# Kernel optimization log

Measured on AMD Instinct MI355X. Metric: run time of the kernel, lower is better.

Reference implementation:

```python
import jax, jax.numpy as jnp
import numpy as np

N = 50000      # nodes
E = 1600000    # edges (avg degree 32)
F_IN = 3       # PROTEINS num_node_features
H = 64         # dim_h
G = 512        # num graphs in batch
C = 2          # PROTEINS num_classes
BN_EPS = 1e-5


def setup_inputs() -> dict:
    key = jax.random.key(0)
    ks = iter(jax.random.split(key, 64))

    def rn(shape, s=0.1):
        return (jax.random.normal(next(ks), shape) * s).astype(jnp.float32)

    inp = {"x": rn((N, F_IN), 1.0)}
    for li, din in ((1, F_IN), (2, H), (3, H)):
        p = f"conv{li}_"
        inp[p + "w1"] = rn((din, H))
        inp[p + "b1"] = rn((H,))
        inp[p + "bn_g"] = jnp.ones((H,), jnp.float32)
        inp[p + "bn_b"] = jnp.zeros((H,), jnp.float32)
        inp[p + "bn_m"] = rn((H,))
        inp[p + "bn_v"] = jax.random.uniform(next(ks), (H,), jnp.float32, 0.5, 1.5)
        inp[p + "w2"] = rn((H, H))
        inp[p + "b2"] = rn((H,))
    inp["lin1_w"] = rn((3 * H, 3 * H))
    inp["lin1_b"] = rn((3 * H,))
    inp["lin2_w"] = rn((3 * H, C))
    inp["lin2_b"] = rn((C,))
    inp["edge_index"] = jax.random.randint(next(ks), (2, E), 0, N, jnp.int64)
    inp["batch"] = jnp.sort(jax.random.randint(next(ks), (N,), 0, G, jnp.int64))
    return inp


def gin_conv(x, src, dst, w1, b1, g, bb, m, v, w2, b2):
    # GINConv, eps=0: mlp(x + sum_{j->i} x_j); aggregate messages at target (dst)
    agg = jax.ops.segment_sum(x[src], dst, num_segments=N)  # [N, d]
    h = x + agg
    h = h @ w1 + b1
    h = (h - m) * jax.lax.rsqrt(v + BN_EPS) * g + bb  # BatchNorm1d (eval)
    h = jax.nn.relu(h)
    h = jax.nn.relu(h @ w2 + b2)
    return h


def reference(x,
              conv1_w1, conv1_b1, conv1_bn_g, conv1_bn_b, conv1_bn_m, conv1_bn_v, conv1_w2, conv1_b2,
              conv2_w1, conv2_b1, conv2_bn_g, conv2_bn_b, conv2_bn_m, conv2_bn_v, conv2_w2, conv2_b2,
              conv3_w1, conv3_b1, conv3_bn_g, conv3_bn_b, conv3_bn_m, conv3_bn_v, conv3_w2, conv3_b2,
              lin1_w, lin1_b, lin2_w, lin2_b,
              edge_index, batch):
    src, dst = edge_index[0], edge_index[1]
    h1 = gin_conv(x,  src, dst, conv1_w1, conv1_b1, conv1_bn_g, conv1_bn_b, conv1_bn_m, conv1_bn_v, conv1_w2, conv1_b2)
    h2 = gin_conv(h1, src, dst, conv2_w1, conv2_b1, conv2_bn_g, conv2_bn_b, conv2_bn_m, conv2_bn_v, conv2_w2, conv2_b2)
    h3 = gin_conv(h2, src, dst, conv3_w1, conv3_b1, conv3_bn_g, conv3_bn_b, conv3_bn_m, conv3_bn_v, conv3_w2, conv3_b2)
    # global_add_pool per graph
    p1 = jax.ops.segment_sum(h1, batch, num_segments=G)
    p2 = jax.ops.segment_sum(h2, batch, num_segments=G)
    p3 = jax.ops.segment_sum(h3, batch, num_segments=G)
    h = jnp.concatenate((p1, p2, p3), axis=1)          # [G, 3H]
    h = jax.nn.relu(h @ lin1_w + lin1_b)
    # dropout p=0.5 is identity in eval mode
    h = h @ lin2_w + lin2_b                            # [G, C]
    return (h, jax.nn.log_softmax(h, axis=1))
```

## Files before the change

### kernel.cpp

```cpp
#include <hip/hip_runtime.h>
#include <hip/hip_bf16.h>
#include <math.h>

#define N_NODES 50000
#define N_EDGES 1600000
#define H 64
#define G_GRAPHS 512
#define C_CLS 2
#define BN_EPS 1e-5f
#define NBUCK 196
#define E4 (N_EDGES / 4)
#define CSR_BLOCKS ((E4 + 511) / 512)

typedef __attribute__((ext_vector_type(8))) short short8;
typedef __attribute__((ext_vector_type(4))) float floatx4;

__device__ __forceinline__ float bflo(unsigned int u) { return __uint_as_float(u << 16); }
__device__ __forceinline__ float bfhi(unsigned int u) { return __uint_as_float(u & 0xffff0000u); }
__device__ __forceinline__ unsigned int bf16_rne(float f) {
    unsigned int u = __float_as_uint(f);
    u += 0x7fffu + ((u >> 16) & 1u);
    return u >> 16;
}

__global__ __launch_bounds__(256) void pack_x_kernel(const float* __restrict__ x,
                                                     uint2* __restrict__ xb) {
    int node = blockIdx.x * blockDim.x + threadIdx.x;
    if (node >= N_NODES) return;
    uint2 p;
    p.x = bf16_rne(x[node * 3 + 0]) | (bf16_rne(x[node * 3 + 1]) << 16);
    p.y = bf16_rne(x[node * 3 + 2]);
    xb[node] = p;
}

__global__ __launch_bounds__(256) void bhist_kernel(const int* __restrict__ dst,
                                                    int* __restrict__ gbh) {
    __shared__ int bh[NBUCK];
    int t = threadIdx.x;
    if (t < NBUCK) bh[t] = 0;
    __syncthreads();
    int base = blockIdx.x * 512;
#pragma unroll
    for (int p = 0; p < 2; p++) {
        int i = base + p * 256 + t;
        if (i < E4) {
            int4 d = ((const int4*)dst)[i];
            atomicAdd(&bh[d.x >> 8], 1);
            atomicAdd(&bh[d.y >> 8], 1);
            atomicAdd(&bh[d.z >> 8], 1);
            atomicAdd(&bh[d.w >> 8], 1);
        }
    }
    __syncthreads();
    if (t < NBUCK && bh[t]) atomicAdd(&gbh[t], bh[t]);
}

__global__ __launch_bounds__(256) void bscan_kernel(const int* __restrict__ gbh,
                                                    int* __restrict__ bucket_start,
                                                    int* __restrict__ cursor,
                                                    int* __restrict__ row_start) {
    __shared__ int s[256];
    int t = threadIdx.x;
    int v = (t < NBUCK) ? gbh[t] : 0;
    s[t] = v;
    __syncthreads();
    for (int off = 1; off < 256; off <<= 1) {
        int u = 0;
        if (t >= off) u = s[t - off];
        __syncthreads();
        if (t >= off) s[t] += u;
        __syncthreads();
    }
    int excl = s[t] - v;
    if (t < NBUCK) { bucket_start[t] = excl; cursor[t] = excl; }
    if (t == 0) { bucket_start[NBUCK] = N_EDGES; row_start[N_NODES] = N_EDGES; }
}

__global__ __launch_bounds__(256) void bscatter_kernel(const int* __restrict__ src,
                                                       const int* __restrict__ dst,
                                                       int* __restrict__ cursor,
                                                       int* __restrict__ gpacked) {
    __shared__ int bh[NBUCK];
    int t = threadIdx.x;
    if (t < NBUCK) bh[t] = 0;
    __syncthreads();
    int base = blockIdx.x * 512;

    int pkA[4], bkA[4], lrA[4]; bool vA = false;
    int pkB[4], bkB[4], lrB[4]; bool vB = false;
    {
        int i = base + t;
        if (i < E4) {
            vA = true;
            int4 s4 = ((const int4*)src)[i];
            int4 d4 = ((const int4*)dst)[i];
            bkA[0] = d4.x >> 8; pkA[0] = ((d4.x & 255) << 16) | s4.x; lrA[0] = atomicAdd(&bh[bkA[0]], 1);
            bkA[1] = d4.y >> 8; pkA[1] = ((d4.y & 255) << 16) | s4.y; lrA[1] = atomicAdd(&bh[bkA[1]], 1);
            bkA[2] = d4.z >> 8; pkA[2] = ((d4.z & 255) << 16) | s4.z; lrA[2] = atomicAdd(&bh[bkA[2]], 1);
            bkA[3] = d4.w >> 8; pkA[3] = ((d4.w & 255) << 16) | s4.w; lrA[3] = atomicAdd(&bh[bkA[3]], 1);
        }
    }
    {
        int i = base + 256 + t;
        if (i < E4) {
            vB = true;
            int4 s4 = ((const int4*)src)[i];
            int4 d4 = ((const int4*)dst)[i];
            bkB[0] = d4.x >> 8; pkB[0] = ((d4.x & 255) << 16) | s4.x; lrB[0] = atomicAdd(&bh[bkB[0]], 1);
            bkB[1] = d4.y >> 8; pkB[1] = ((d4.y & 255) << 16) | s4.y; lrB[1] = atomicAdd(&bh[bkB[1]], 1);
            bkB[2] = d4.z >> 8; pkB[2] = ((d4.z & 255) << 16) | s4.z; lrB[2] = atomicAdd(&bh[bkB[2]], 1);
            bkB[3] = d4.w >> 8; pkB[3] = ((d4.w & 255) << 16) | s4.w; lrB[3] = atomicAdd(&bh[bkB[3]], 1);
        }
    }
    __syncthreads();
    if (t < NBUCK) {
        int c = bh[t];
        bh[t] = c ? atomicAdd(&cursor[t], c) : 0;
    }
    __syncthreads();
    if (vA) {
#pragma unroll
        for (int q = 0; q < 4; q++) gpacked[bh[bkA[q]] + lrA[q]] = pkA[q];
    }
    if (vB) {
#pragma unroll
        for (int q = 0; q < 4; q++) gpacked[bh[bkB[q]] + lrB[q]] = pkB[q];
    }
}

__global__ __launch_bounds__(256) void bcsr_kernel(const int* __restrict__ gpacked,
                                                   const int* __restrict__ bucket_start,
                                                   int* __restrict__ row_start,
                                                   int* __restrict__ edge_src) {
    __shared__ int cnt[256];
    __shared__ int pref[256];
    int b = blockIdx.x;
    int t = threadIdx.x;
    int bs = bucket_start[b], be = bucket_start[b + 1];
    cnt[t] = 0;
    __syncthreads();
    for (int i = bs + t; i < be; i += 256) atomicAdd(&cnt[gpacked[i] >> 16], 1);
    __syncthreads();
    int v = cnt[t];
    pref[t] = v;
    __syncthreads();
    for (int off = 1; off < 256; off <<= 1) {
        int u = 0;
        if (t >= off) u = pref[t - off];
        __syncthreads();
        if (t >= off) pref[t] += u;
        __syncthreads();
    }
    int excl = pref[t] - v;
    int node = b * 256 + t;
    if (node < N_NODES) row_start[node] = bs + excl;
    cnt[t] = excl;
    __syncthreads();
    for (int i = bs + t; i < be; i += 256) {
        int p = gpacked[i];
        int pos = atomicAdd(&cnt[p >> 16], 1);
        edge_src[bs + pos] = p & 0xffff;
    }
}

__global__ __launch_bounds__(512) void gather3_mid_kernel(
    const float* __restrict__ x, const uint2* __restrict__ xb,
    const int* __restrict__ row_start, const int* __restrict__ edge_src,
    const float* __restrict__ w1, const float* __restrict__ b1,
    const float* __restrict__ bn_g, const float* __restrict__ bn_b,
    const float* __restrict__ bn_m, const float* __restrict__ bn_v,
    __hip_bfloat16* __restrict__ mid) {
    int tid = threadIdx.x;
    int wave = tid >> 6;
    int j = tid & 63;
    int node = blockIdx.x * 8 + wave;

    int rs = row_start[node], re = row_start[node + 1];
    float a0 = 0.f, a1 = 0.f, a2 = 0.f;
    for (int t = rs + j; t < re; t += 64) {
        uint2 p = xb[edge_src[t]];
        a0 += bflo(p.x);
        a1 += bfhi(p.x);
        a2 += bflo(p.y);
    }
#pragma unroll
    for (int off = 32; off > 0; off >>= 1) {
        a0 += __shfl_xor(a0, off);
        a1 += __shfl_xor(a1, off);
        a2 += __shfl_xor(a2, off);
    }
    float in0 = a0 + x[node * 3 + 0];
    float in1 = a1 + x[node * 3 + 1];
    float in2 = a2 + x[node * 3 + 2];

    float sc = rsqrtf(bn_v[j] + BN_EPS) * bn_g[j];
    float sh = bn_b[j] - bn_m[j] * sc;
    float m = b1[j] + in0 * w1[j] + in1 * w1[H + j] + in2 * w1[2 * H + j];
    m = fmaxf(m * sc + sh, 0.f);
    ((unsigned short*)mid)[(size_t)node * H + j] = (unsigned short)bf16_rne(m);
}

#define IOP 72
__global__ __launch_bounds__(256) void matmul2_mfma_kernel(
    const __hip_bfloat16* __restrict__ xin,
    const float* __restrict__ w2, const float* __restrict__ b2,
    __hip_bfloat16* __restrict__ hout) {
    __shared__ unsigned short s_w2t[H * IOP];
    __shared__ unsigned short s_out[4][16 * IOP];

    int tid = threadIdx.x;
    for (int idx = tid; idx < H * H; idx += 256) {
        int k = idx >> 6, jj = idx & 63;
        s_w2t[jj * IOP + k] = (unsigned short)bf16_rne(w2[idx]);
    }
    int lane = tid & 63, wave = tid >> 6;
    int quad = lane >> 4, l15 = lane & 15;
    float bb2[4];
#pragma unroll
    for (int jt = 0; jt < 4; jt++) bb2[jt] = b2[jt * 16 + l15];
    __syncthreads();

    int base = blockIdx.x * 64 + wave * 16;
    const unsigned short* xr = (const unsigned short*)xin;
    int am = min(base + l15, N_NODES - 1);
    short8 a0 = *(const short8*)(xr + (size_t)am * H + quad * 8);
    short8 a1 = *(const short8*)(xr + (size_t)am * H + quad * 8 + 32);

    unsigned short* outw = s_out[wave];
#pragma unroll
    for (int jt = 0; jt < 4; jt++) {
        short8 b0 = *(const short8*)&s_w2t[(jt * 16 + l15) * IOP + quad * 8];
        short8 bv = *(const short8*)&s_w2t[(jt * 16 + l15) * IOP + quad * 8 + 32];
        floatx4 c = {0.f, 0.f, 0.f, 0.f};
        c = __builtin_amdgcn_mfma_f32_16x16x32_bf16(a0, b0, c, 0, 0, 0);
        c = __builtin_amdgcn_mfma_f32_16x16x32_bf16(a1, bv, c, 0, 0, 0);
#pragma unroll
        for (int r = 0; r < 4; r++) {
            float v = fmaxf(c[r] + bb2[jt], 0.f);
            outw[(quad * 4 + r) * IOP + jt * 16 + l15] = (unsigned short)bf16_rne(v);
        }
    }
    __syncthreads();

    unsigned short* ho = (unsigned short*)hout;
#pragma unroll
    for (int cc = 0; cc < 2; cc++) {
        int r = cc * 8 + (lane >> 3);
        int node = base + r;
        if (node < N_NODES) {
            short8 v = *(const short8*)&outw[r * IOP + (lane & 7) * 8];
            *(short8*)(ho + (size_t)node * H + (lane & 7) * 8) = v;
        }
    }
}

__global__ __launch_bounds__(512) void gather_kernel(
    const __hip_bfloat16* __restrict__ hin, const int* __restrict__ row_start,
    const int* __restrict__ edge_src, __hip_bfloat16* __restrict__ xs) {
    int tid = threadIdx.x;
    int wave = tid >> 6;
    int j = tid & 63;
    int o = j >> 3;
    int jo = j & 7;
    int node = blockIdx.x * 8 + wave;

    const char* hb = (const char*)hin;
    int rs = row_start[node], re = row_start[node + 1];
    float a0 = 0.f, a1 = 0.f, a2 = 0.f, a3 = 0.f, a4 = 0.f, a5 = 0.f, a6 = 0.f, a7 = 0.f;
    for (int base = rs; base < re; base += 64) {
        int idx = base + j;
        int sv = (idx < re) ? edge_src[idx] : 0;
        int cnt = min(64, re - base);
        int i = 0;
        for (; i + 8 <= cnt; i += 8) {
            int s = __shfl(sv, i + o);
            uint4 raw = *(const uint4*)(hb + (size_t)s * 128 + jo * 16);
            a0 += bflo(raw.x); a1 += bfhi(raw.x);
            a2 += bflo(raw.y); a3 += bfhi(raw.y);
            a4 += bflo(raw.z); a5 += bfhi(raw.z);
            a6 += bflo(raw.w); a7 += bfhi(raw.w);
        }
        if (i < cnt) {
            int r = cnt - i;
            int s = __shfl(sv, i + (o < r ? o : 0));
            uint4 raw = *(const uint4*)(hb + (size_t)s * 128 + jo * 16);
            if (o < r) {
                a0 += bflo(raw.x); a1 += bfhi(raw.x);
                a2 += bflo(raw.y); a3 += bfhi(raw.y);
                a4 += bflo(raw.z); a5 += bfhi(raw.z);
                a6 += bflo(raw.w); a7 += bfhi(raw.w);
            }
        }
    }
    a0 += __shfl_xor(a0, 8); a0 += __shfl_xor(a0, 16); a0 += __shfl_xor(a0, 32);
    a1 += __shfl_xor(a1, 8); a1 += __shfl_xor(a1, 16); a1 += __shfl_xor(a1, 32);
    a2 += __shfl_xor(a2, 8); a2 += __shfl_xor(a2, 16); a2 += __shfl_xor(a2, 32);
    a3 += __shfl_xor(a3, 8); a3 += __shfl_xor(a3, 16); a3 += __shfl_xor(a3, 32);
    a4 += __shfl_xor(a4, 8); a4 += __shfl_xor(a4, 16); a4 += __shfl_xor(a4, 32);
    a5 += __shfl_xor(a5, 8); a5 += __shfl_xor(a5, 16); a5 += __shfl_xor(a5, 32);
    a6 += __shfl_xor(a6, 8); a6 += __shfl_xor(a6, 16); a6 += __shfl_xor(a6, 32);
    a7 += __shfl_xor(a7, 8); a7 += __shfl_xor(a7, 16); a7 += __shfl_xor(a7, 32);
    if (o == 0) {
        uint4 raw = *(const uint4*)(hb + (size_t)node * 128 + jo * 16);
        a0 += bflo(raw.x); a1 += bfhi(raw.x);
        a2 += bflo(raw.y); a3 += bfhi(raw.y);
        a4 += bflo(raw.z); a5 += bfhi(raw.z);
        a6 += bflo(raw.w); a7 += bfhi(raw.w);
        uint4 ov;
        ov.x = bf16_rne(a0) | (bf16_rne(a1) << 16);
        ov.y = bf16_rne(a2) | (bf16_rne(a3) << 16);
        ov.z = bf16_rne(a4) | (bf16_rne(a5) << 16);
        ov.w = bf16_rne(a6) | (bf16_rne(a7) << 16);
        *(uint4*)((char*)xs + (size_t)node * 128 + jo * 16) = ov;
    }
}

__global__ __launch_bounds__(256) void mlp_mfma_kernel(
    const __hip_bfloat16* __restrict__ xs,
    const float* __restrict__ w1, const float* __restrict__ b1,
    const float* __restrict__ bn_g, const float* __restrict__ bn_b,
    const float* __restrict__ bn_m, const float* __restrict__ bn_v,
    const float* __restrict__ w2, const float* __restrict__ b2,
    __hip_bfloat16* __restrict__ hout) {
    __shared__ unsigned short s_w1t[H * IOP];
    __shared__ unsigned short s_w2t[H * IOP];
    __shared__ unsigned short s_mid[4][16 * IOP];
    __shared__ unsigned short s_out[4][16 * IOP];

    int tid = threadIdx.x;
    for (int idx = tid; idx < H * H; idx += 256) {
        int k = idx >> 6, jj = idx & 63;
        s_w1t[jj * IOP + k] = (unsigned short)bf16_rne(w1[idx]);
        s_w2t[jj * IOP + k] = (unsigned short)bf16_rne(w2[idx]);
    }
    int lane = tid & 63, wave = tid >> 6;
    int quad = lane >> 4, l15 = lane & 15;
    float scl[4], sht[4], bb1[4], bb2[4];
#pragma unroll
    for (int jt = 0; jt < 4; jt++) {
        int j = jt * 16 + l15;
        float sc = rsqrtf(bn_v[j] + BN_EPS) * bn_g[j];
        scl[jt] = sc;
        sht[jt] = bn_b[j] - bn_m[j] * sc;
        bb1[jt] = b1[j];
        bb2[jt] = b2[j];
    }
    __syncthreads();

    int base = blockIdx.x * 64 + wave * 16;
    const unsigned short* xr = (const unsigned short*)xs;
    int am = min(base + l15, N_NODES - 1);
    short8 a0 = *(const short8*)(xr + (size_t)am * H + quad * 8);
    short8 a1 = *(const short8*)(xr + (size_t)am * H + quad * 8 + 32);

    unsigned short* mid = s_mid[wave];
    unsigned short* outw = s_out[wave];

#pragma unroll
    for (int jt = 0; jt < 4; jt++) {
        short8 b0 = *(const short8*)&s_w1t[(jt * 16 + l15) * IOP + quad * 8];
        short8 bv = *(const short8*)&s_w1t[(jt * 16 + l15) * IOP + quad * 8 + 32];
        floatx4 c = {0.f, 0.f, 0.f, 0.f};
        c = __builtin_amdgcn_mfma_f32_16x16x32_bf16(a0, b0, c, 0, 0, 0);
        c = __builtin_amdgcn_mfma_f32_16x16x32_bf16(a1, bv, c, 0, 0, 0);
#pragma unroll
        for (int r = 0; r < 4; r++) {
            float v = (c[r] + bb1[jt]) * scl[jt] + sht[jt];
            v = fmaxf(v, 0.f);
            mid[(quad * 4 + r) * IOP + jt * 16 + l15] = (unsigned short)bf16_rne(v);
        }
    }
    __syncthreads();

    short8 m0 = *(const short8*)&mid[l15 * IOP + quad * 8];
    short8 m1 = *(const short8*)&mid[l15 * IOP + quad * 8 + 32];
#pragma unroll
    for (int jt = 0; jt < 4; jt++) {
        short8 b0 = *(const short8*)&s_w2t[(jt * 16 + l15) * IOP + quad * 8];
        short8 bv = *(const short8*)&s_w2t[(jt * 16 + l15) * IOP + quad * 8 + 32];
        floatx4 c = {0.f, 0.f, 0.f, 0.f};
        c = __builtin_amdgcn_mfma_f32_16x16x32_bf16(m0, b0, c, 0, 0, 0);
        c = __builtin_amdgcn_mfma_f32_16x16x32_bf16(m1, bv, c, 0, 0, 0);
#pragma unroll
        for (int r = 0; r < 4; r++) {
            float v = fmaxf(c[r] + bb2[jt], 0.f);
            outw[(quad * 4 + r) * IOP + jt * 16 + l15] = (unsigned short)bf16_rne(v);
        }
    }
    __syncthreads();

    unsigned short* ho = (unsigned short*)hout;
#pragma unroll
    for (int cc = 0; cc < 2; cc++) {
        int r = cc * 8 + (lane >> 3);
        int node = base + r;
        if (node < N_NODES) {
            short8 v = *(const short8*)&outw[r * IOP + (lane & 7) * 8];
            *(short8*)(ho + (size_t)node * H + (lane & 7) * 8) = v;
        }
    }
}

__global__ __launch_bounds__(192) void pool_head_kernel(
    const __hip_bfloat16* __restrict__ h1, const __hip_bfloat16* __restrict__ h2,
    const __hip_bfloat16* __restrict__ h3, const int* __restrict__ batch,
    const float* __restrict__ lin1_w, const float* __restrict__ lin1_b,
    const float* __restrict__ lin2_w, const float* __restrict__ lin2_b,
    float* __restrict__ out) {
    __shared__ float s_row[3 * H];
    __shared__ float s_mid[3 * H];
    __shared__ float s_z[C_CLS];
    __shared__ int s_se[2];

    int g = blockIdx.x;
    int j = threadIdx.x;
    if (j < 2) {
        int target = g + j;
        int lo = 0, hi = N_NODES;
        while (lo < hi) {
            int mid = (lo + hi) >> 1;
            if (batch[mid] < target) lo = mid + 1; else hi = mid;
        }
        s_se[j] = lo;
    }
    __syncthreads();
    int ns = s_se[0], ne = s_se[1];

    int which = j >> 6;
    int f = j & 63;
    const __hip_bfloat16* h = (which == 0) ? h1 : ((which == 1) ? h2 : h3);
    float p0 = 0.f, p1 = 0.f, p2 = 0.f, p3 = 0.f;
    int n = ns;
    for (; n + 3 < ne; n += 4) {
        p0 += __bfloat162float(h[(size_t)n * H + f]);
        p1 += __bfloat162float(h[(size_t)(n + 1) * H + f]);
        p2 += __bfloat162float(h[(size_t)(n + 2) * H + f]);
        p3 += __bfloat162float(h[(size_t)(n + 3) * H + f]);
    }
    for (; n < ne; n++) p0 += __bfloat162float(h[(size_t)n * H + f]);
    s_row[j] = (p0 + p1) + (p2 + p3);
    __syncthreads();

    float acc = lin1_b[j];
    for (int k = 0; k < 3 * H; k++) acc += s_row[k] * lin1_w[k * (3 * H) + j];
    s_mid[j] = fmaxf(acc, 0.f);
    __syncthreads();

    if (j < C_CLS) {
        float z = lin2_b[j];
        for (int k = 0; k < 3 * H; k++) z += s_mid[k] * lin2_w[k * C_CLS + j];
        s_z[j] = z;
    }
    __syncthreads();
    if (j < C_CLS) {
        float z0 = s_z[0], z1 = s_z[1];
        float mx = fmaxf(z0, z1);
        float lse = mx + logf(expf(z0 - mx) + expf(z1 - mx));
        out[g * C_CLS + j] = s_z[j];
        out[G_GRAPHS * C_CLS + g * C_CLS + j] = s_z[j] - lse;
    }
}

extern "C" void kernel_launch(void* const* d_in, const int* in_sizes, int n_in,
                              void* d_out, int out_size, void* d_ws, size_t ws_size,
                              hipStream_t stream) {
    const float* x = (const float*)d_in[0];
    const float* cw1[3], *cb1[3], *cg[3], *cbb[3], *cm[3], *cv[3], *cw2[3], *cb2[3];
    for (int l = 0; l < 3; l++) {
        int b = 1 + 8 * l;
        cw1[l] = (const float*)d_in[b + 0];
        cb1[l] = (const float*)d_in[b + 1];
        cg[l]  = (const float*)d_in[b + 2];
        cbb[l] = (const float*)d_in[b + 3];
        cm[l]  = (const float*)d_in[b + 4];
        cv[l]  = (const float*)d_in[b + 5];
        cw2[l] = (const float*)d_in[b + 6];
        cb2[l] = (const float*)d_in[b + 7];
    }
    const float* lin1_w = (const float*)d_in[25];
    const float* lin1_b = (const float*)d_in[26];
    const float* lin2_w = (const float*)d_in[27];
    const float* lin2_b = (const float*)d_in[28];
    const int* edge_index = (const int*)d_in[29];
    const int* batch = (const int*)d_in[30];
    const int* src = edge_index;
    const int* dst = edge_index + N_EDGES;
    float* out = (float*)d_out;

    int* edge_src = (int*)d_ws;
    int* gpacked = edge_src + N_EDGES;
    int* gbh = gpacked + N_EDGES;
    int* bucket_start = gbh + NBUCK;
    int* cursor = bucket_start + NBUCK + 1;
    int* row_start = cursor + NBUCK;
    uintptr_t hp = (uintptr_t)(row_start + N_NODES + 2);
    hp = (hp + 127) & ~(uintptr_t)127;
    uint2* xb = (uint2*)hp;
    __hip_bfloat16* h1 = (__hip_bfloat16*)(xb + N_NODES);
    __hip_bfloat16* h2 = h1 + (size_t)N_NODES * H;
    __hip_bfloat16* h3 = h2 + (size_t)N_NODES * H;
    __hip_bfloat16* xs = h3 + (size_t)N_NODES * H;

    hipMemsetAsync(gbh, 0, NBUCK * sizeof(int), stream);
    pack_x_kernel<<<(N_NODES + 255) / 256, 256, 0, stream>>>(x, xb);
    bhist_kernel<<<CSR_BLOCKS, 256, 0, stream>>>(dst, gbh);
    bscan_kernel<<<1, 256, 0, stream>>>(gbh, bucket_start, cursor, row_start);
    bscatter_kernel<<<CSR_BLOCKS, 256, 0, stream>>>(src, dst, cursor, gpacked);
    bcsr_kernel<<<NBUCK, 256, 0, stream>>>(gpacked, bucket_start, row_start, edge_src);

    const int mlp_grid = (N_NODES + 63) / 64;

    gather3_mid_kernel<<<N_NODES / 8, 512, 0, stream>>>(x, xb, row_start, edge_src,
        cw1[0], cb1[0], cg[0], cbb[0], cm[0], cv[0], xs);
    matmul2_mfma_kernel<<<mlp_grid, 256, 0, stream>>>(xs, cw2[0], cb2[0], h1);
    gather_kernel<<<N_NODES / 8, 512, 0, stream>>>(h1, row_start, edge_src, xs);
    mlp_mfma_kernel<<<mlp_grid, 256, 0, stream>>>(xs,
        cw1[1], cb1[1], cg[1], cbb[1], cm[1], cv[1], cw2[1], cb2[1], h2);
    gather_kernel<<<N_NODES / 8, 512, 0, stream>>>(h2, row_start, edge_src, xs);
    mlp_mfma_kernel<<<mlp_grid, 256, 0, stream>>>(xs,
        cw1[2], cb1[2], cg[2], cbb[2], cm[2], cv[2], cw2[2], cb2[2], h3);
    pool_head_kernel<<<G_GRAPHS, 3 * H, 0, stream>>>(h1, h2, h3, batch,
        lin1_w, lin1_b, lin2_w, lin2_b, out);
}
```

Baseline: 315.2 us.

## Fuse neighbor gather with GIN MLP per wave and pretranspose weights once

Each GIN layer's gather kernel and MFMA MLP kernel are merged into one kernel. Each wave gathers 16 nodes into shared memory and then runs both matmuls on that tile, so the intermediate xs buffer no longer makes a global round trip. This also cuts launches from six to three. The weight transpose and bf16 conversion move into a single prep kernel that writes to a workspace, and the fused kernels read B fragments straight from global memory instead of staging them in LDS. The trade-off is that each wave now runs 16 nodes serially, with fewer blocks and less parallelism per node. The unpadded global weight reads may also hit the cache less efficiently.

```diff
diff --git a/kernel.cpp b/kernel.cpp
--- a/kernel.cpp
+++ b/kernel.cpp
@@ -11,6 +11,8 @@
 #define NBUCK 196
 #define E4 (N_EDGES / 4)
 #define CSR_BLOCKS ((E4 + 511) / 512)
+#define IOP 72
+#define NPB 128
 
 typedef __attribute__((ext_vector_type(8))) short short8;
 typedef __attribute__((ext_vector_type(4))) float floatx4;
@@ -23,14 +25,29 @@
     return u >> 16;
 }
 
-__global__ __launch_bounds__(256) void pack_x_kernel(const float* __restrict__ x,
-                                                     uint2* __restrict__ xb) {
-    int node = blockIdx.x * blockDim.x + threadIdx.x;
-    if (node >= N_NODES) return;
-    uint2 p;
-    p.x = bf16_rne(x[node * 3 + 0]) | (bf16_rne(x[node * 3 + 1]) << 16);
-    p.y = bf16_rne(x[node * 3 + 2]);
-    xb[node] = p;
+__global__ __launch_bounds__(256) void prep_kernel(
+    const float* __restrict__ w2_0, const float* __restrict__ w1_1,
+    const float* __restrict__ w2_1, const float* __restrict__ w1_2,
+    const float* __restrict__ w2_2, unsigned short* __restrict__ wt,
+    const float* __restrict__ x, uint2* __restrict__ xb) {
+    int b = blockIdx.x, t = threadIdx.x;
+    if (b < 5) {
+        const float* w = (b == 0) ? w2_0 : (b == 1) ? w1_1 : (b == 2) ? w2_1
+                         : (b == 3) ? w1_2 : w2_2;
+        unsigned short* o = wt + b * (H * H);
+        for (int idx = t; idx < H * H; idx += 256) {
+            int k = idx >> 6, j = idx & 63;
+            o[j * H + k] = (unsigned short)bf16_rne(w[idx]);
+        }
+    } else {
+        int node = (b - 5) * 256 + t;
+        if (node < N_NODES) {
+            uint2 p;
+            p.x = bf16_rne(x[node * 3 + 0]) | (bf16_rne(x[node * 3 + 1]) << 16);
+            p.y = bf16_rne(x[node * 3 + 2]);
+            xb[node] = p;
+        }
+    }
 }
 
 __global__ __launch_bounds__(256) void bhist_kernel(const int* __restrict__ dst,
@@ -163,203 +180,173 @@
     }
 }
 
-__global__ __launch_bounds__(512) void gather3_mid_kernel(
+__global__ __launch_bounds__(512) void gin1_fused_kernel(
     const float* __restrict__ x, const uint2* __restrict__ xb,
     const int* __restrict__ row_start, const int* __restrict__ edge_src,
     const float* __restrict__ w1, const float* __restrict__ b1,
     const float* __restrict__ bn_g, const float* __restrict__ bn_b,
     const float* __restrict__ bn_m, const float* __restrict__ bn_v,
-    __hip_bfloat16* __restrict__ mid) {
+    const unsigned short* __restrict__ w2t, const float* __restrict__ b2,
+    __hip_bfloat16* __restrict__ hout) {
+    __shared__ unsigned short s_mid[8][16 * IOP];
+    __shared__ unsigned short s_out[8][16 * IOP];
+
     int tid = threadIdx.x;
-    int wave = tid >> 6;
-    int j = tid & 63;
-    int node = blockIdx.x * 8 + wave;
-
-    int rs = row_start[node], re = row_start[node + 1];
-    float a0 = 0.f, a1 = 0.f, a2 = 0.f;
-    for (int t = rs + j; t < re; t += 64) {
-        uint2 p = xb[edge_src[t]];
-        a0 += bflo(p.x);
-        a1 += bfhi(p.x);
-        a2 += bflo(p.y);
-    }
-#pragma unroll
-    for (int off = 32; off > 0; off >>= 1) {
-        a0 += __shfl_xor(a0, off);
-        a1 += __shfl_xor(a1, off);
-        a2 += __shfl_xor(a2, off);
-    }
-    float in0 = a0 + x[node * 3 + 0];
-    float in1 = a1 + x[node * 3 + 1];
-    float in2 = a2 + x[node * 3 + 2];
-
+    int wave = tid >> 6, j = tid & 63;
+    int quad = j >> 4, l15 = j & 15;
+    int nodebase = blockIdx.x * NPB + wave * 16;
+
+    float wj0 = w1[j], wj1 = w1[H + j], wj2 = w1[2 * H + j];
     float sc = rsqrtf(bn_v[j] + BN_EPS) * bn_g[j];
     float sh = bn_b[j] - bn_m[j] * sc;
-    float m = b1[j] + in0 * w1[j] + in1 * w1[H + j] + in2 * w1[2 * H + j];
-    m = fmaxf(m * sc + sh, 0.f);
-    ((unsigned short*)mid)[(size_t)node * H + j] = (unsigned short)bf16_rne(m);
-}
-
-#define IOP 72
-__global__ __launch_bounds__(256) void matmul2_mfma_kernel(
-    const __hip_bfloat16* __restrict__ xin,
-    const float* __restrict__ w2, const float* __restrict__ b2,
-    __hip_bfloat16* __restrict__ hout) {
-    __shared__ unsigned short s_w2t[H * IOP];
-    __shared__ unsigned short s_out[4][16 * IOP];
-
-    int tid = threadIdx.x;
-    for (int idx = tid; idx < H * H; idx += 256) {
-        int k = idx >> 6, jj = idx & 63;
-        s_w2t[jj * IOP + k] = (unsigned short)bf16_rne(w2[idx]);
-    }
-    int lane = tid & 63, wave = tid >> 6;
-    int quad = lane >> 4, l15 = lane & 15;
+    float bj = b1[j];
     float bb2[4];
 #pragma unroll
     for (int jt = 0; jt < 4; jt++) bb2[jt] = b2[jt * 16 + l15];
-    __syncthreads();
-
-    int base = blockIdx.x * 64 + wave * 16;
-    const unsigned short* xr = (const unsigned short*)xin;
-    int am = min(base + l15, N_NODES - 1);
-    short8 a0 = *(const short8*)(xr + (size_t)am * H + quad * 8);
-    short8 a1 = *(const short8*)(xr + (size_t)am * H + quad * 8 + 32);
-
+
+    unsigned short* mid = s_mid[wave];
     unsigned short* outw = s_out[wave];
+
+    for (int nl = 0; nl < 16; nl++) {
+        int node = min(nodebase + nl, N_NODES - 1);
+        int rs = row_start[node], re = row_start[node + 1];
+        float a0 = 0.f, a1 = 0.f, a2 = 0.f;
+        for (int t = rs + j; t < re; t += 64) {
+            uint2 p = xb[edge_src[t]];
+            a0 += bflo(p.x); a1 += bfhi(p.x); a2 += bflo(p.y);
+        }
+#pragma unroll
+        for (int off = 32; off > 0; off >>= 1) {
+            a0 += __shfl_xor(a0, off);
+            a1 += __shfl_xor(a1, off);
+            a2 += __shfl_xor(a2, off);
+        }
+        float in0 = a0 + x[node * 3 + 0];
+        float in1 = a1 + x[node * 3 + 1];
+        float in2 = a2 + x[node * 3 + 2];
+        float m = bj + in0 * wj0 + in1 * wj1 + in2 * wj2;
+        m = fmaxf(m * sc + sh, 0.f);
+        mid[nl * IOP + j] = (unsigned short)bf16_rne(m);
+    }
+
+    short8 m0 = *(const short8*)&mid[l15 * IOP + quad * 8];
+    short8 m1 = *(const short8*)&mid[l15 * IOP + quad * 8 + 32];
 #pragma unroll
     for (int jt = 0; jt < 4; jt++) {
-        short8 b0 = *(const short8*)&s_w2t[(jt * 16 + l15) * IOP + quad * 8];
-        short8 bv = *(const short8*)&s_w2t[(jt * 16 + l15) * IOP + quad * 8 + 32];
+        short8 b0 = *(const short8*)&w2t[(jt * 16 + l15) * H + quad * 8];
+        short8 bv = *(const short8*)&w2t[(jt * 16 + l15) * H + quad * 8 + 32];
         floatx4 c = {0.f, 0.f, 0.f, 0.f};
-        c = __builtin_amdgcn_mfma_f32_16x16x32_bf16(a0, b0, c, 0, 0, 0);
-        c = __builtin_amdgcn_mfma_f32_16x16x32_bf16(a1, bv, c, 0, 0, 0);
+        c = __builtin_amdgcn_mfma_f32_16x16x32_bf16(m0, b0, c, 0, 0, 0);
+        c = __builtin_amdgcn_mfma_f32_16x16x32_bf16(m1, bv, c, 0, 0, 0);
 #pragma unroll
         for (int r = 0; r < 4; r++) {
             float v = fmaxf(c[r] + bb2[jt], 0.f);
             outw[(quad * 4 + r) * IOP + jt * 16 + l15] = (unsigned short)bf16_rne(v);
         }
     }
-    __syncthreads();
 
     unsigned short* ho = (unsigned short*)hout;
 #pragma unroll
     for (int cc = 0; cc < 2; cc++) {
-        int r = cc * 8 + (lane >> 3);
-        int node = base + r;
+        int r = cc * 8 + (j >> 3);
+        int node = nodebase + r;
         if (node < N_NODES) {
-            short8 v = *(const short8*)&outw[r * IOP + (lane & 7) * 8];
-            *(short8*)(ho + (size_t)node * H + (lane & 7) * 8) = v;
-        }
-    }
-}
-
-__global__ __launch_bounds__(512) void gather_kernel(
+            short8 v = *(const short8*)&outw[r * IOP + (j & 7) * 8];
+            *(short8*)(ho + (size_t)node * H + (j & 7) * 8) = v;
+        }
+    }
+}
+
+__global__ __launch_bounds__(512) void gin_fused_kernel(
     const __hip_bfloat16* __restrict__ hin, const int* __restrict__ row_start,
-    const int* __restrict__ edge_src, __hip_bfloat16* __restrict__ xs) {
+    const int* __restrict__ edge_src,
+    const unsigned short* __restrict__ w1t, const float* __restrict__ b1,
+    const float* __restrict__ bn_g, const float* __restrict__ bn_b,
+    const float* __restrict__ bn_m, const float* __restrict__ bn_v,
+    const unsigned short* __restrict__ w2t, const float* __restrict__ b2,
+    __hip_bfloat16* __restrict__ hout) {
+    __shared__ unsigned short s_xs[8][16 * IOP];
+    __shared__ unsigned short s_mid[8][16 * IOP];
+
     int tid = threadIdx.x;
-    int wave = tid >> 6;
-    int j = tid & 63;
-    int o = j >> 3;
-    int jo = j & 7;
-    int node = blockIdx.x * 8 + wave;
-
+    int wave = tid >> 6, j = tid & 63;
+    int o = j >> 3, jo = j & 7;
+    int quad = j >> 4, l15 = j & 15;
+    int nodebase = blockIdx.x * NPB + wave * 16;
+
+    float scl[4], sht[4], bb1[4], bb2[4];
+#pragma unroll
+    for (int jt = 0; jt < 4; jt++) {
+        int jj = jt * 16 + l15;
+        float sc = rsqrtf(bn_v[jj] + BN_EPS) * bn_g[jj];
+        scl[jt] = sc;
+        sht[jt] = bn_b[jj] - bn_m[jj] * sc;
+        bb1[jt] = b1[jj];
+        bb2[jt] = b2[jj];
+    }
+
+    unsigned short* xsw = s_xs[wave];
+    unsigned short* mid = s_mid[wave];
     const char* hb = (const char*)hin;
-    int rs = row_start[node], re = row_start[node + 1];
-    float a0 = 0.f, a1 = 0.f, a2 = 0.f, a3 = 0.f, a4 = 0.f, a5 = 0.f, a6 = 0.f, a7 = 0.f;
-    for (int base = rs; base < re; base += 64) {
-        int idx = base + j;
-        int sv = (idx < re) ? edge_src[idx] : 0;
-        int cnt = min(64, re - base);
-        int i = 0;
-        for (; i + 8 <= cnt; i += 8) {
-            int s = __shfl(sv, i + o);
-            uint4 raw = *(const uint4*)(hb + (size_t)s * 128 + jo * 16);
-            a0 += bflo(raw.x); a1 += bfhi(raw.x);
-            a2 += bflo(raw.y); a3 += bfhi(raw.y);
-            a4 += bflo(raw.z); a5 += bfhi(raw.z);
-            a6 += bflo(raw.w); a7 += bfhi(raw.w);
-        }
-        if (i < cnt) {
-            int r = cnt - i;
-            int s = __shfl(sv, i + (o < r ? o : 0));
-            uint4 raw = *(const uint4*)(hb + (size_t)s * 128 + jo * 16);
-            if (o < r) {
+
+    for (int nl = 0; nl < 16; nl++) {
+        int node = min(nodebase + nl, N_NODES - 1);
+        int rs = row_start[node], re = row_start[node + 1];
+        float a0 = 0.f, a1 = 0.f, a2 = 0.f, a3 = 0.f, a4 = 0.f, a5 = 0.f, a6 = 0.f, a7 = 0.f;
+        for (int base = rs; base < re; base += 64) {
+            int idx = base + j;
+            int sv = (idx < re) ? edge_src[idx] : 0;
+            int cnt = min(64, re - base);
+            int i = 0;
+            for (; i + 8 <= cnt; i += 8) {
+                int s = __shfl(sv, i + o);
+                uint4 raw = *(const uint4*)(hb + (size_t)s * 128 + jo * 16);
                 a0 += bflo(raw.x); a1 += bfhi(raw.x);
                 a2 += bflo(raw.y); a3 += bfhi(raw.y);
                 a4 += bflo(raw.z); a5 += bfhi(raw.z);
                 a6 += bflo(raw.w); a7 += bfhi(raw.w);
             }
-        }
-    }
-    a0 += __shfl_xor(a0, 8); a0 += __shfl_xor(a0, 16); a0 += __shfl_xor(a0, 32);
-    a1 += __shfl_xor(a1, 8); a1 += __shfl_xor(a1, 16); a1 += __shfl_xor(a1, 32);
-    a2 += __shfl_xor(a2, 8); a2 += __shfl_xor(a2, 16); a2 += __shfl_xor(a2, 32);
-    a3 += __shfl_xor(a3, 8); a3 += __shfl_xor(a3, 16); a3 += __shfl_xor(a3, 32);
-    a4 += __shfl_xor(a4, 8); a4 += __shfl_xor(a4, 16); a4 += __shfl_xor(a4, 32);
-    a5 += __shfl_xor(a5, 8); a5 += __shfl_xor(a5, 16); a5 += __shfl_xor(a5, 32);
-    a6 += __shfl_xor(a6, 8); a6 += __shfl_xor(a6, 16); a6 += __shfl_xor(a6, 32);
-    a7 += __shfl_xor(a7, 8); a7 += __shfl_xor(a7, 16); a7 += __shfl_xor(a7, 32);
-    if (o == 0) {
-        uint4 raw = *(const uint4*)(hb + (size_t)node * 128 + jo * 16);
-        a0 += bflo(raw.x); a1 += bfhi(raw.x);
-        a2 += bflo(raw.y); a3 += bfhi(raw.y);
-        a4 += bflo(raw.z); a5 += bfhi(raw.z);
-        a6 += bflo(raw.w); a7 += bfhi(raw.w);
-        uint4 ov;
-        ov.x = bf16_rne(a0) | (bf16_rne(a1) << 16);
-        ov.y = bf16_rne(a2) | (bf16_rne(a3) << 16);
-        ov.z = bf16_rne(a4) | (bf16_rne(a5) << 16);
-        ov.w = bf16_rne(a6) | (bf16_rne(a7) << 16);
-        *(uint4*)((char*)xs + (size_t)node * 128 + jo * 16) = ov;
-    }
-}
-
-__global__ __launch_bounds__(256) void mlp_mfma_kernel(
-    const __hip_bfloat16* __restrict__ xs,
-    const float* __restrict__ w1, const float* __restrict__ b1,
-    const float* __restrict__ bn_g, const float* __restrict__ bn_b,
-    const float* __restrict__ bn_m, const float* __restrict__ bn_v,
-    const float* __restrict__ w2, const float* __restrict__ b2,
-    __hip_bfloat16* __restrict__ hout) {
-    __shared__ unsigned short s_w1t[H * IOP];
-    __shared__ unsigned short s_w2t[H * IOP];
-    __shared__ unsigned short s_mid[4][16 * IOP];
-    __shared__ unsigned short s_out[4][16 * IOP];
-
-    int tid = threadIdx.x;
-    for (int idx = tid; idx < H * H; idx += 256) {
-        int k = idx >> 6, jj = idx & 63;
-        s_w1t[jj * IOP + k] = (unsigned short)bf16_rne(w1[idx]);
-        s_w2t[jj * IOP + k] = (unsigned short)bf16_rne(w2[idx]);
-    }
-    int lane = tid & 63, wave = tid >> 6;
-    int quad = lane >> 4, l15 = lane & 15;
-    float scl[4], sht[4], bb1[4], bb2[4];
+            if (i < cnt) {
+                int r = cnt - i;
+                int s = __shfl(sv, i + (o < r ? o : 0));
+                uint4 raw = *(const uint4*)(hb + (size_t)s * 128 + jo * 16);
+                if (o < r) {
+                    a0 += bflo(raw.x); a1 += bfhi(raw.x);
+                    a2 += bflo(raw.y); a3 += bfhi(raw.y);
+                    a4 += bflo(raw.z); a5 += bfhi(raw.z);
+                    a6 += bflo(raw.w); a7 += bfhi(raw.w);
+                }
+            }
+        }
+        a0 += __shfl_xor(a0, 8); a0 += __shfl_xor(a0, 16); a0 += __shfl_xor(a0, 32);
+        a1 += __shfl_xor(a1, 8); a1 += __shfl_xor(a1, 16); a1 += __shfl_xor(a1, 32);
+        a2 += __shfl_xor(a2, 8); a2 += __shfl_xor(a2, 16); a2 += __shfl_xor(a2, 32);
+        a3 += __shfl_xor(a3, 8); a3 += __shfl_xor(a3, 16); a3 += __shfl_xor(a3, 32);
+        a4 += __shfl_xor(a4, 8); a4 += __shfl_xor(a4, 16); a4 += __shfl_xor(a4, 32);
+        a5 += __shfl_xor(a5, 8); a5 += __shfl_xor(a5, 16); a5 += __shfl_xor(a5, 32);
+        a6 += __shfl_xor(a6, 8); a6 += __shfl_xor(a6, 16); a6 += __shfl_xor(a6, 32);
+        a7 += __shfl_xor(a7, 8); a7 += __shfl_xor(a7, 16); a7 += __shfl_xor(a7, 32);
+        if (o == 0) {
+            uint4 raw = *(const uint4*)(hb + (size_t)node * 128 + jo * 16);
+            a0 += bflo(raw.x); a1 += bfhi(raw.x);
+            a2 += bflo(raw.y); a3 += bfhi(raw.y);
+            a4 += bflo(raw.z); a5 += bfhi(raw.z);
+            a6 += bflo(raw.w); a7 += bfhi(raw.w);
+            uint4 ov;
+            ov.x = bf16_rne(a0) | (bf16_rne(a1) << 16);
+            ov.y = bf16_rne(a2) | (bf16_rne(a3) << 16);
+            ov.z = bf16_rne(a4) | (bf16_rne(a5) << 16);
+            ov.w = bf16_rne(a6) | (bf16_rne(a7) << 16);
+            *(uint4*)&xsw[nl * IOP + jo * 8] = ov;
+        }
+    }
+
+    short8 a0 = *(const short8*)&xsw[l15 * IOP + quad * 8];
+    short8 a1 = *(const short8*)&xsw[l15 * IOP + quad * 8 + 32];
 #pragma unroll
     for (int jt = 0; jt < 4; jt++) {
-        int j = jt * 16 + l15;
-        float sc = rsqrtf(bn_v[j] + BN_EPS) * bn_g[j];
-        scl[jt] = sc;
-        sht[jt] = bn_b[j] - bn_m[j] * sc;
-        bb1[jt] = b1[j];
-        bb2[jt] = b2[j];
-    }
-    __syncthreads();
-
-    int base = blockIdx.x * 64 + wave * 16;
-    const unsigned short* xr = (const unsigned short*)xs;
-    int am = min(base + l15, N_NODES - 1);
-    short8 a0 = *(const short8*)(xr + (size_t)am * H + quad * 8);
-    short8 a1 = *(const short8*)(xr + (size_t)am * H + quad * 8 + 32);
-
-    unsigned short* mid = s_mid[wave];
-    unsigned short* outw = s_out[wave];
-
-#pragma unroll
-    for (int jt = 0; jt < 4; jt++) {
-        short8 b0 = *(const short8*)&s_w1t[(jt * 16 + l15) * IOP + quad * 8];
-        short8 bv = *(const short8*)&s_w1t[(jt * 16 + l15) * IOP + quad * 8 + 32];
+        short8 b0 = *(const short8*)&w1t[(jt * 16 + l15) * H + quad * 8];
+        short8 bv = *(const short8*)&w1t[(jt * 16 + l15) * H + quad * 8 + 32];
         floatx4 c = {0.f, 0.f, 0.f, 0.f};
         c = __builtin_amdgcn_mfma_f32_16x16x32_bf16(a0, b0, c, 0, 0, 0);
         c = __builtin_amdgcn_mfma_f32_16x16x32_bf16(a1, bv, c, 0, 0, 0);
@@ -370,33 +357,31 @@
             mid[(quad * 4 + r) * IOP + jt * 16 + l15] = (unsigned short)bf16_rne(v);
         }
     }
-    __syncthreads();
 
     short8 m0 = *(const short8*)&mid[l15 * IOP + quad * 8];
     short8 m1 = *(const short8*)&mid[l15 * IOP + quad * 8 + 32];
 #pragma unroll
     for (int jt = 0; jt < 4; jt++) {
-        short8 b0 = *(const short8*)&s_w2t[(jt * 16 + l15) * IOP + quad * 8];
-        short8 bv = *(const short8*)&s_w2t[(jt * 16 + l15) * IOP + quad * 8 + 32];
+        short8 b0 = *(const short8*)&w2t[(jt * 16 + l15) * H + quad * 8];
+        short8 bv = *(const short8*)&w2t[(jt * 16 + l15) * H + quad * 8 + 32];
         floatx4 c = {0.f, 0.f, 0.f, 0.f};
         c = __builtin_amdgcn_mfma_f32_16x16x32_bf16(m0, b0, c, 0, 0, 0);
         c = __builtin_amdgcn_mfma_f32_16x16x32_bf16(m1, bv, c, 0, 0, 0);
 #pragma unroll
         for (int r = 0; r < 4; r++) {
             float v = fmaxf(c[r] + bb2[jt], 0.f);
-            outw[(quad * 4 + r) * IOP + jt * 16 + l15] = (unsigned short)bf16_rne(v);
-        }
-    }
-    __syncthreads();
+            xsw[(quad * 4 + r) * IOP + jt * 16 + l15] = (unsigned short)bf16_rne(v);
+        }
+    }
 
     unsigned short* ho = (unsigned short*)hout;
 #pragma unroll
     for (int cc = 0; cc < 2; cc++) {
-        int r = cc * 8 + (lane >> 3);
-        int node = base + r;
+        int r = cc * 8 + (j >> 3);
+        int node = nodebase + r;
         if (node < N_NODES) {
-            short8 v = *(const short8*)&outw[r * IOP + (lane & 7) * 8];
-            *(short8*)(ho + (size_t)node * H + (lane & 7) * 8) = v;
+            short8 v = *(const short8*)&xsw[r * IOP + (j & 7) * 8];
+            *(short8*)(ho + (size_t)node * H + (j & 7) * 8) = v;
         }
     }
 }
@@ -495,30 +480,34 @@
     int* row_start = cursor + NBUCK;
     uintptr_t hp = (uintptr_t)(row_start + N_NODES + 2);
     hp = (hp + 127) & ~(uintptr_t)127;
-    uint2* xb = (uint2*)hp;
+    unsigned short* wt = (unsigned short*)hp;
+    uint2* xb = (uint2*)(wt + 5 * H * H);
     __hip_bfloat16* h1 = (__hip_bfloat16*)(xb + N_NODES);
     __hip_bfloat16* h2 = h1 + (size_t)N_NODES * H;
     __hip_bfloat16* h3 = h2 + (size_t)N_NODES * H;
-    __hip_bfloat16* xs = h3 + (size_t)N_NODES * H;
+
+    const unsigned short* w2t_0 = wt + 0 * H * H;
+    const unsigned short* w1t_1 = wt + 1 * H * H;
+    const unsigned short* w2t_1 = wt + 2 * H * H;
+    const unsigned short* w1t_2 = wt + 3 * H * H;
+    const unsigned short* w2t_2 = wt + 4 * H * H;
 
     hipMemsetAsync(gbh, 0, NBUCK * sizeof(int), stream);
-    pack_x_kernel<<<(N_NODES + 255) / 256, 256, 0, stream>>>(x, xb);
+    prep_kernel<<<5 + (N_NODES + 255) / 256, 256, 0, stream>>>(
+        cw2[0], cw1[1], cw2[1], cw1[2], cw2[2], wt, x, xb);
     bhist_kernel<<<CSR_BLOCKS, 256, 0, stream>>>(dst, gbh);
     bscan_kernel<<<1, 256, 0, stream>>>(gbh, bucket_start, cursor, row_start);
     bscatter_kernel<<<CSR_BLOCKS, 256, 0, stream>>>(src, dst, cursor, gpacked);
     bcsr_kernel<<<NBUCK, 256, 0, stream>>>(gpacked, bucket_start, row_start, edge_src);
 
-    const int mlp_grid = (N_NODES + 63) / 64;
-
-    gather3_mid_kernel<<<N_NODES / 8, 512, 0, stream>>>(x, xb, row_start, edge_src,
-        cw1[0], cb1[0], cg[0], cbb[0], cm[0], cv[0], xs);
-    matmul2_mfma_kernel<<<mlp_grid, 256, 0, stream>>>(xs, cw2[0], cb2[0], h1);
-    gather_kernel<<<N_NODES / 8, 512, 0, stream>>>(h1, row_start, edge_src, xs);
-    mlp_mfma_kernel<<<mlp_grid, 256, 0, stream>>>(xs,
-        cw1[1], cb1[1], cg[1], cbb[1], cm[1], cv[1], cw2[1], cb2[1], h2);
-    gather_kernel<<<N_NODES / 8, 512, 0, stream>>>(h2, row_start, edge_src, xs);
-    mlp_mfma_kernel<<<mlp_grid, 256, 0, stream>>>(xs,
-        cw1[2], cb1[2], cg[2], cbb[2], cm[2], cv[2], cw2[2], cb2[2], h3);
+    const int fgrid = (N_NODES + NPB - 1) / NPB;
+
+    gin1_fused_kernel<<<fgrid, 512, 0, stream>>>(x, xb, row_start, edge_src,
+        cw1[0], cb1[0], cg[0], cbb[0], cm[0], cv[0], w2t_0, cb2[0], h1);
+    gin_fused_kernel<<<fgrid, 512, 0, stream>>>(h1, row_start, edge_src,
+        w1t_1, cb1[1], cg[1], cbb[1], cm[1], cv[1], w2t_1, cb2[1], h2);
+    gin_fused_kernel<<<fgrid, 512, 0, stream>>>(h2, row_start, edge_src,
+        w1t_2, cb1[2], cg[2], cbb[2], cm[2], cv[2], w2t_2, cb2[2], h3);
     pool_head_kernel<<<G_GRAPHS, 3 * H, 0, stream>>>(h1, h2, h3, batch,
         lin1_w, lin1_b, lin2_w, lin2_b, out);
 }
```

Result: slower. 361.2 us (+14.6%).
